# Kernel optimization log

Hardware: AMD Instinct MI355X
Metric: run time of the kernel (lower is better)

## Reference

```python
import jax, jax.numpy as jnp
import numpy as np

B, N, C = 4, 262144, 10
K_PRE, K_POST = 4096, 500          # before_nms_max, after_nms_max
ROI_THR, NMS_THR = 0.1, 0.01       # roi_threshold, nms_threshold


def setup_inputs() -> dict:
    key = jax.random.key(0)
    k1, k2, k3, k4 = jax.random.split(key, 4)
    # raw logits; sigmoid(-2 + noise) straddles roi_threshold=0.1 realistically
    cls = jax.random.normal(k1, (B, N, C), jnp.float32) - 2.0
    centers = jax.random.uniform(k2, (B, N, 3), jnp.float32, minval=-50.0, maxval=50.0)
    sizes = jax.random.uniform(k3, (B, N, 3), jnp.float32, minval=0.5, maxval=5.0)
    heading = jax.random.uniform(k4, (B, N, 1), jnp.float32, minval=-np.pi, maxval=np.pi)
    boxes = jnp.concatenate([centers, sizes, heading], axis=-1)  # (B, N, 7)
    return {"batch_cls_preds": cls, "batch_box_preds": boxes}


def _pairwise_bev_iou(b):
    # b: (K, 7) = [x, y, z, dx, dy, dz, heading]; BEV IoU (heading ignored,
    # axis-aligned approximation of the rotated-IoU CUDA kernel).
    x, y, dx, dy = b[:, 0], b[:, 1], b[:, 3], b[:, 4]
    x1, x2 = x - dx * 0.5, x + dx * 0.5
    y1, y2 = y - dy * 0.5, y + dy * 0.5
    ix = jnp.clip(jnp.minimum(x2[:, None], x2[None, :]) - jnp.maximum(x1[:, None], x1[None, :]), 0.0)
    iy = jnp.clip(jnp.minimum(y2[:, None], y2[None, :]) - jnp.maximum(y1[:, None], y1[None, :]), 0.0)
    inter = ix * iy                              # (K, K)
    area = dx * dy                               # (K,)
    union = area[:, None] + area[None, :] - inter
    return inter / jnp.maximum(union, 1e-6)


def _nms_one(scores, labels, boxes):
    # scores: (N,), labels: (N,) int32, boxes: (N, 7)
    s = jnp.where(scores > ROI_THR, scores, -1.0)       # score-threshold filter
    topv, topi = jax.lax.top_k(s, K_PRE)                # keep top before_nms_max
    tb = boxes[topi]                                     # (K_PRE, 7)
    tl = labels[topi]
    iou = _pairwise_bev_iou(tb)                          # (K_PRE, K_PRE)
    keep0 = topv > ROI_THR

    def body(i, keep):
        # a kept higher-score box i suppresses later boxes with IoU > thr
        sup = (iou[i] > NMS_THR) & (jnp.arange(K_PRE) > i) & keep[i]
        return keep & ~sup

    keep = jax.lax.fori_loop(0, K_PRE, body, keep0)
    kept_scores = jnp.where(keep, topv, -1.0)
    fv, fi = jax.lax.top_k(kept_scores, K_POST)          # after_nms_max slots
    m = fv > 0.0
    final_scores = jnp.where(m, fv, 0.0)                 # (K_POST,)
    final_boxes = tb[fi] * m[:, None].astype(tb.dtype)   # (K_POST, 7)
    final_labels = jnp.where(m, tl[fi], -1)              # (K_POST,)
    return final_scores, final_boxes, final_labels


def reference(batch_cls_preds, batch_box_preds):
    probs = jax.nn.sigmoid(batch_cls_preds)              # (B, N, C)
    scores = jnp.max(probs, axis=-1)                     # per-anchor best class score
    labels = jnp.argmax(probs, axis=-1).astype(jnp.int32)
    final_scores, final_boxes, final_labels = jax.vmap(_nms_one)(scores, labels, batch_box_preds)
    return final_scores, final_boxes, final_labels
```

## Files before the change

### kernel.cpp

```cpp
#include <hip/hip_runtime.h>
#include <stdint.h>

constexpr int B = 4;
constexpr int N = 262144;
constexpr int C = 10;
constexpr int KPRE = 4096;
constexpr int KPOST = 500;
constexpr float ROI_THR = 0.1f;
constexpr float NMS_THR = 0.01f;
constexpr int CAP = 8192;
constexpr int MASKW = KPRE / 64;
constexpr int RJT = 2;

__device__ __forceinline__ uint32_t f2k(float f) {
  uint32_t u = __float_as_uint(f);
  return (u & 0x80000000u) ? ~u : (u | 0x80000000u);
}
__device__ __forceinline__ float k2f(uint32_t k) {
  uint32_t u = (k & 0x80000000u) ? (k ^ 0x80000000u) : ~k;
  return __uint_as_float(u);
}
__device__ __forceinline__ float sigm(float x) { return 1.0f / (1.0f + expf(-x)); }

__device__ __forceinline__ void async_lds16(const void* g, void* l) {
  __builtin_amdgcn_global_load_lds((const __attribute__((address_space(1))) void*)g,
                                   (__attribute__((address_space(3))) void*)l, 16, 0, 0);
}

__device__ __forceinline__ uint2 select256(const uint32_t* __restrict__ h, uint32_t R,
                                           uint32_t* s, uint32_t* o2) {
  int t = threadIdx.x;
  s[t] = h[t];
  __syncthreads();
  for (int off = 1; off < 256; off <<= 1) {
    uint32_t v = s[t] + ((t + off < 256) ? s[t + off] : 0u);
    __syncthreads();
    s[t] = v;
    __syncthreads();
  }
  uint32_t suf = s[t];
  uint32_t sufn = (t < 255) ? s[t + 1] : 0u;
  if (suf >= R && R > sufn) {
    o2[0] = (uint32_t)t;
    o2[1] = R - sufn;
  }
  __syncthreads();
  uint2 r;
  r.x = o2[0];
  r.y = o2[1];
  __syncthreads();
  return r;
}

__global__ void scoreK(const float* __restrict__ cls, uint32_t* __restrict__ keys,
                       uint32_t* __restrict__ hist0) {
  __shared__ float ls[2560];
  __shared__ uint32_t h[256];
  int b = blockIdx.y;
  int t = threadIdx.x;
  h[t] = 0;
  size_t base = ((size_t)b * N + (size_t)blockIdx.x * 256) * C;
  const float2* g2 = (const float2*)(cls + base);
  float2* l2 = (float2*)ls;
#pragma unroll
  for (int r = 0; r < 5; ++r) l2[r * 256 + t] = g2[r * 256 + t];
  __syncthreads();
  const float* mine = ls + t * 10;
  float m = mine[0];
#pragma unroll
  for (int c = 1; c < C; ++c) m = fmaxf(m, mine[c]);
  float p = sigm(m);
  float sc = (p > ROI_THR) ? p : -1.0f;
  uint32_t k = f2k(sc);
  keys[(size_t)b * N + blockIdx.x * 256 + t] = k;
  atomicAdd(&h[k >> 24], 1u);
  __syncthreads();
  if (h[t]) atomicAdd(&hist0[b * 256 + t], h[t]);
}

__global__ void histP1K(const uint32_t* __restrict__ keys, const uint32_t* __restrict__ hist0,
                        uint32_t* __restrict__ hist1) {
  __shared__ uint32_t s[256];
  __shared__ uint32_t o2[2];
  __shared__ uint32_t h[256];
  int b = blockIdx.y;
  int t = threadIdx.x;
  uint2 s0 = select256(hist0 + b * 256, (uint32_t)KPRE, s, o2);
  h[t] = 0;
  __syncthreads();
  uint32_t pref = s0.x;
  const uint4* kb4 = (const uint4*)(keys + (size_t)b * N);
#pragma unroll
  for (int r = 0; r < 2; ++r) {
    uint4 kv = kb4[blockIdx.x * 512 + r * 256 + t];
#pragma unroll
    for (int j = 0; j < 4; ++j) {
      uint32_t k = (&kv.x)[j];
      if ((k >> 24) == pref) atomicAdd(&h[(k >> 16) & 255u], 1u);
    }
  }
  __syncthreads();
  if (h[t]) atomicAdd(&hist1[b * 256 + t], h[t]);
}

__global__ void compactK(const uint32_t* __restrict__ keys, const uint32_t* __restrict__ hist0,
                         const uint32_t* __restrict__ hist1, unsigned long long* __restrict__ list,
                         uint32_t* __restrict__ cnt) {
  __shared__ uint32_t s[256];
  __shared__ uint32_t o2[2];
  __shared__ uint32_t scan[256];
  __shared__ uint32_t baseSh;
  int b = blockIdx.y;
  int t = threadIdx.x;
  uint2 s0 = select256(hist0 + b * 256, (uint32_t)KPRE, s, o2);
  uint2 s1 = select256(hist1 + b * 256, s0.y, s, o2);
  uint32_t T = ((s0.x << 8) | s1.x) << 16;
  const uint4* kb4 = (const uint4*)(keys + (size_t)b * N);
  uint4 kv[4];
#pragma unroll
  for (int r = 0; r < 4; ++r) kv[r] = kb4[blockIdx.x * 1024 + r * 256 + t];
  uint32_t c = 0;
#pragma unroll
  for (int r = 0; r < 4; ++r)
#pragma unroll
    for (int j = 0; j < 4; ++j) c += ((&kv[r].x)[j] >= T) ? 1u : 0u;
  scan[t] = c;
  __syncthreads();
  for (int off = 1; off < 256; off <<= 1) {
    uint32_t v = scan[t] + ((t >= off) ? scan[t - off] : 0u);
    __syncthreads();
    scan[t] = v;
    __syncthreads();
  }
  uint32_t excl = scan[t] - c;
  if (t == 255) baseSh = atomicAdd(&cnt[b], scan[255]);
  __syncthreads();
  uint32_t pos = baseSh + excl;
#pragma unroll
  for (int r = 0; r < 4; ++r)
#pragma unroll
    for (int j = 0; j < 4; ++j) {
      uint32_t k = (&kv[r].x)[j];
      if (k >= T) {
        uint32_t n = (blockIdx.x * 1024 + r * 256 + t) * 4 + j;
        if (pos < CAP)
          list[(size_t)b * CAP + pos] = ((unsigned long long)k << 32) | (uint32_t)(~n);
        pos++;
      }
    }
}

__global__ void rankK(const unsigned long long* __restrict__ list, const uint32_t* __restrict__ cnt,
                      uint32_t* __restrict__ rank) {
  __shared__ unsigned long long lp[256];
  int b = blockIdx.z;
  int cc = (int)min(cnt[b], (uint32_t)CAP);
  if (blockIdx.x * 256 >= cc) return;
  int j0 = blockIdx.y * (256 * RJT);
  if (j0 >= cc) return;
  int i = blockIdx.x * 256 + threadIdx.x;
  unsigned long long pi = (i < cc) ? list[(size_t)b * CAP + i] : ~0ull;
  uint32_t c = 0;
#pragma unroll
  for (int tb = 0; tb < RJT; ++tb) {
    int j = j0 + tb * 256 + threadIdx.x;
    __syncthreads();
    lp[threadIdx.x] = (j < cc) ? list[(size_t)b * CAP + j] : 0ull;
    __syncthreads();
#pragma unroll 8
    for (int jj = 0; jj < 256; ++jj) c += (lp[jj] > pi) ? 1u : 0u;
  }
  if (i < cc && c) atomicAdd(&rank[(size_t)b * CAP + i], c);
}

__global__ void scatterK(const unsigned long long* __restrict__ list,
                         const uint32_t* __restrict__ cnt, const uint32_t* __restrict__ rank,
                         const float* __restrict__ boxes, float* __restrict__ sel_score,
                         uint32_t* __restrict__ sel_idx, float* __restrict__ sel_box) {
  int b = blockIdx.y;
  int p = blockIdx.x * 256 + threadIdx.x;
  uint32_t cc = min(cnt[b], (uint32_t)CAP);
  if (p >= (int)cc) return;
  unsigned long long pk = list[(size_t)b * CAP + p];
  uint32_t r = rank[(size_t)b * CAP + p];
  if (r >= (uint32_t)KPRE) return;
  uint32_t key = (uint32_t)(pk >> 32);
  uint32_t idx = ~(uint32_t)pk;
  sel_score[b * KPRE + r] = k2f(key);
  sel_idx[b * KPRE + r] = idx;
  const float* src = boxes + ((size_t)b * N + idx) * 7;
  float* dst = sel_box + ((size_t)b * KPRE + r) * 8;
#pragma unroll
  for (int c = 0; c < 7; ++c) dst[c] = src[c];
  dst[7] = 0.f;
}

__global__ void maskK(const float* __restrict__ sel_box, unsigned long long* __restrict__ mask) {
  int b = blockIdx.z;
  int bi = blockIdx.x;
  int w = blockIdx.y;
  int t = threadIdx.x;
  int i = bi * 256 + t;
  int j0 = w * 64;
  unsigned long long* dst = mask + ((size_t)b * KPRE + i) * MASKW + w;
  if (j0 + 63 <= bi * 256) {
    *dst = 0ull;
    return;
  }
  __shared__ float4 jv[64];
  __shared__ float ja[64];
  if (t < 64) {
    const float4* bj = (const float4*)(sel_box + ((size_t)b * KPRE + j0 + t) * 8);
    float4 lo = bj[0], hi = bj[1];
    float xj = lo.x, yj = lo.y, dxj = lo.w, dyj = hi.x;
    float hxj = __fmul_rn(dxj, 0.5f), hyj = __fmul_rn(dyj, 0.5f);
    float4 v;
    v.x = __fsub_rn(xj, hxj);
    v.y = __fadd_rn(xj, hxj);
    v.z = __fsub_rn(yj, hyj);
    v.w = __fadd_rn(yj, hyj);
    jv[t] = v;
    ja[t] = __fmul_rn(dxj, dyj);
  }
  __syncthreads();
  const float4* myb = (const float4*)(sel_box + ((size_t)b * KPRE + i) * 8);
  float4 lo = myb[0], hi = myb[1];
  float x = lo.x, y = lo.y, dx = lo.w, dy = hi.x;
  float hx = __fmul_rn(dx, 0.5f), hy = __fmul_rn(dy, 0.5f);
  float x1i = __fsub_rn(x, hx), x2i = __fadd_rn(x, hx);
  float y1i = __fsub_rn(y, hy), y2i = __fadd_rn(y, hy);
  float ai = __fmul_rn(dx, dy);
  unsigned long long wacc = 0ull;
#pragma unroll 16
  for (int jj = 0; jj < 64; ++jj) {
    int j = j0 + jj;
    float4 v = jv[jj];
    float aj = ja[jj];
    float xx1 = fmaxf(x1i, v.x);
    float xx2 = fminf(x2i, v.y);
    float yy1 = fmaxf(y1i, v.z);
    float yy2 = fminf(y2i, v.w);
    float ix = fmaxf(__fsub_rn(xx2, xx1), 0.0f);
    float iy = fmaxf(__fsub_rn(yy2, yy1), 0.0f);
    float inter = __fmul_rn(ix, iy);
    float den = fmaxf(__fsub_rn(__fadd_rn(ai, aj), inter), 1e-6f);
    float q0 = __fmul_rn(NMS_THR, den);
    float d = __fsub_rn(inter, q0);
    bool sup = d > 0.0f;
    if (__builtin_expect(__any(fabsf(d) <= q0 * 1e-5f), 0)) {
      sup = (inter / den) > NMS_THR;
    }
    sup = sup && (j > i);
    wacc |= ((unsigned long long)(sup ? 1u : 0u)) << jj;
  }
  *dst = wacc;
}

__global__ void transK(const unsigned long long* __restrict__ mask,
                       unsigned long long* __restrict__ Tmat) {
  int b = blockIdx.y;
  int g = blockIdx.x;
  int t = threadIdx.x;
  unsigned long long m = mask[((size_t)b * KPRE + g * 64 + t) * MASKW + g];
  unsigned long long T = 0ull;
#pragma unroll
  for (int j = 0; j < 64; ++j) {
    unsigned long long bj = __ballot(((m >> j) & 1ull) != 0ull);
    if (t == j) T = bj;
  }
  Tmat[((size_t)b * 64 + g) * 128 + t] = T;
  Tmat[((size_t)b * 64 + g) * 128 + 64 + t] = m;
}

__global__ void nmsK(const unsigned long long* __restrict__ mask,
                     const unsigned long long* __restrict__ Tmat,
                     const float* __restrict__ sel_score,
                     uint32_t* __restrict__ kept_pos, uint32_t* __restrict__ kept_cnt) {
  __shared__ unsigned long long lds[3][64][64];
  __shared__ unsigned long long tl[3][128];
  __shared__ uint32_t keptbuf[KPOST];
  int b = blockIdx.x;
  int t = threadIdx.x;

  unsigned long long cand = 0ull;
  for (int k = 0; k < 64; ++k) {
    float s = sel_score[b * KPRE + k * 64 + t];
    unsigned long long bal = __ballot(s > ROI_THR);
    if (t == k) cand = bal;
  }

  const unsigned long long* mb = mask + (size_t)b * KPRE * MASKW;
  const unsigned long long* tb = Tmat + (size_t)b * 64 * 128;
  unsigned long long remv = 0ull;
  int kc = 0;

  auto prefetch = [&](int g2, int buf2) {
    const char* base = (const char*)(mb + (size_t)g2 * 64 * MASKW);
#pragma unroll
    for (int p = 0; p < 32; ++p)
      async_lds16(base + (size_t)p * 1024 + (size_t)t * 16, &lds[buf2][p * 2][0]);
    async_lds16((const char*)(tb + (size_t)g2 * 128) + (size_t)t * 16, &tl[buf2][0]);
  };

  prefetch(0, 0);
  prefetch(1, 1);
  for (int g = 0; g < 64; ++g) {
    int buf = g % 3;
    if (g < 63) {
      asm volatile("s_waitcnt vmcnt(33)" ::: "memory");
    } else {
      asm volatile("s_waitcnt vmcnt(0)" ::: "memory");
    }
    if (g + 2 < 64) {
      asm volatile("s_waitcnt lgkmcnt(0)" ::: "memory");
      prefetch(g + 2, (g + 2) % 3);
    }

    unsigned long long cw = cand & ~remv;
    unsigned long long aw =
        ((unsigned long long)(uint32_t)__builtin_amdgcn_readlane((uint32_t)(cw >> 32), g) << 32) |
        (uint32_t)__builtin_amdgcn_readlane((uint32_t)cw, g);
    if (aw) {
      unsigned long long T = tl[buf][t];
      unsigned long long m = tl[buf][64 + t];
      unsigned long long K = __ballot((m & aw) != 0ull);
      unsigned long long alive = aw;
      unsigned long long rem = aw & K;
      if (rem) {
        bool deadf = ((aw >> t) & 1ull) == 0ull;
        while (rem) {
          int s = __ffsll((long long)rem) - 1;
          rem &= rem - 1ull;
          if ((alive >> s) & 1ull) {
            deadf = deadf || (((T >> s) & 1ull) != 0ull);
            alive = __ballot(!deadf);
            rem &= alive;
          }
        }
      }
      int grp = __popcll(alive);
      if ((alive >> t) & 1ull) {
        int rk = __popcll(alive & ((1ull << t) - 1ull));
        if (kc + rk < KPOST) keptbuf[kc + rk] = (uint32_t)(g * 64 + t);
      }
      unsigned long long acc = 0ull, a2 = alive;
      while (a2) {
        int s2 = __ffsll((long long)a2) - 1;
        a2 &= a2 - 1ull;
        acc |= lds[buf][s2][t];
      }
      remv |= acc;
      kc += grp;
      if (kc >= KPOST) break;
    }
  }
  asm volatile("s_waitcnt vmcnt(0)" ::: "memory");
  int kcc = min(kc, KPOST);
  for (int i = t; i < kcc; i += 64) kept_pos[b * KPOST + i] = keptbuf[i];
  if (t == 0) kept_cnt[b] = (uint32_t)kcc;
}

__global__ void outK(const float* __restrict__ cls,
                     const float* __restrict__ sel_score, const uint32_t* __restrict__ sel_idx,
                     const float* __restrict__ sel_box,
                     const uint32_t* __restrict__ kept_pos, const uint32_t* __restrict__ kept_cnt,
                     float* __restrict__ out) {
  int b = blockIdx.y;
  int s = blockIdx.x * blockDim.x + threadIdx.x;
  if (s >= KPOST) return;
  float* oS = out;
  float* oB = out + B * KPOST;
  float* oL = out + B * KPOST + B * KPOST * 7;
  uint32_t kcnt = kept_cnt[b];
  if (s < (int)kcnt) {
    uint32_t pos = kept_pos[b * KPOST + s];
    oS[b * KPOST + s] = sel_score[b * KPRE + pos];
    const float* box = sel_box + ((size_t)b * KPRE + pos) * 8;
    float* dst = oB + ((size_t)b * KPOST + s) * 7;
#pragma unroll
    for (int c = 0; c < 7; ++c) dst[c] = box[c];
    uint32_t idx = sel_idx[b * KPRE + pos];
    const float* p = cls + ((size_t)b * N + idx) * C;
    float bestv = sigm(p[0]);
    int bestc = 0;
#pragma unroll
    for (int c = 1; c < C; ++c) {
      float v = sigm(p[c]);
      if (v > bestv) { bestv = v; bestc = c; }
    }
    oL[b * KPOST + s] = (float)bestc;
  } else {
    oS[b * KPOST + s] = 0.0f;
    float* dst = oB + ((size_t)b * KPOST + s) * 7;
#pragma unroll
    for (int c = 0; c < 7; ++c) dst[c] = 0.0f;
    oL[b * KPOST + s] = -1.0f;
  }
}

__global__ void sentinelK(float* out, int n) {
  int i = blockIdx.x * blockDim.x + threadIdx.x;
  if (i < n) out[i] = 1337.0f;
}

extern "C" void kernel_launch(void* const* d_in, const int* in_sizes, int n_in,
                              void* d_out, int out_size, void* d_ws, size_t ws_size,
                              hipStream_t stream) {
  const float* cls = (const float*)d_in[0];
  const float* boxes = (const float*)d_in[1];
  float* out = (float*)d_out;

  char* ws = (char*)d_ws;
  size_t off = 0;
  auto alloc = [&](size_t bytes) -> void* {
    void* p = ws + off;
    off = (off + bytes + 255) & ~(size_t)255;
    return p;
  };
  unsigned long long* mask = (unsigned long long*)alloc((size_t)B * KPRE * MASKW * 8);
  unsigned long long* list = (unsigned long long*)alloc((size_t)B * CAP * 8);
  uint32_t* keys = (uint32_t*)alloc((size_t)B * N * 4);
  float* sel_box = (float*)alloc((size_t)B * KPRE * 8 * 4);
  float* sel_score = (float*)alloc((size_t)B * KPRE * 4);
  uint32_t* sel_idx = (uint32_t*)alloc((size_t)B * KPRE * 4);
  uint32_t* kept_pos = (uint32_t*)alloc((size_t)B * KPOST * 4);
  uint32_t* kept_cnt = (uint32_t*)alloc(B * 4);
  unsigned long long* Tmat = (unsigned long long*)alloc((size_t)B * 64 * 128 * 8);

  uint32_t* hist0 = (uint32_t*)mask;
  uint32_t* hist1 = hist0 + B * 256;
  uint32_t* cnt = hist1 + B * 256;
  uint32_t* rank = (uint32_t*)((char*)mask + 16384);
  size_t zbytes = 16384 + (size_t)B * CAP * 4;

  if (off > ws_size) {
    sentinelK<<<dim3((out_size + 255) / 256), 256, 0, stream>>>(out, out_size);
    return;
  }

  hipMemsetAsync(mask, 0, zbytes, stream);
  scoreK<<<dim3(N / 256, B), 256, 0, stream>>>(cls, keys, hist0);
  histP1K<<<dim3(N / 2048, B), 256, 0, stream>>>(keys, hist0, hist1);
  compactK<<<dim3(N / 4096, B), 256, 0, stream>>>(keys, hist0, hist1, list, cnt);
  rankK<<<dim3(CAP / 256, CAP / (256 * RJT), B), 256, 0, stream>>>(list, cnt, rank);
  scatterK<<<dim3(CAP / 256, B), 256, 0, stream>>>(list, cnt, rank, boxes, sel_score, sel_idx,
                                                   sel_box);
  maskK<<<dim3(16, 64, B), 256, 0, stream>>>(sel_box, mask);
  transK<<<dim3(64, B), 64, 0, stream>>>(mask, Tmat);
  nmsK<<<B, 64, 0, stream>>>(mask, Tmat, sel_score, kept_pos, kept_cnt);
  outK<<<dim3((KPOST + 255) / 256, B), 256, 0, stream>>>(cls, sel_score, sel_idx, sel_box,
                                                         kept_pos, kept_cnt, out);
}
```

Baseline: 158.2 us.

## Fuse diagonal transpose into mask kernel and defer NMS row loads into registers

The separate transpose kernel is removed: the mask kernel block that owns each diagonal 64x64 tile now builds the transposed tile with ballots and writes it to Tmat directly. The NMS kernel preloads all diagonal tiles into LDS up front. It replaces the triple-buffered LDS prefetch of whole 64-row mask groups with direct global loads of only the rows of surviving boxes. Those loads go into up to 32 registers and are OR-reduced at the start of the next group, so their latency overlaps the next group's work. This drops one launch and avoids moving unused mask rows. In exchange the serial NMS loop now waits on global-load latency, and the 32-entry register array raises register pressure.

```diff
diff --git a/kernel.cpp b/kernel.cpp
--- a/kernel.cpp
+++ b/kernel.cpp
@@ -11,6 +11,7 @@
 constexpr int CAP = 8192;
 constexpr int MASKW = KPRE / 64;
 constexpr int RJT = 2;
+constexpr int MAXP = 32;
 
 __device__ __forceinline__ uint32_t f2k(float f) {
   uint32_t u = __float_as_uint(f);
@@ -195,7 +196,8 @@
   dst[7] = 0.f;
 }
 
-__global__ void maskK(const float* __restrict__ sel_box, unsigned long long* __restrict__ mask) {
+__global__ void maskK(const float* __restrict__ sel_box, unsigned long long* __restrict__ mask,
+                      unsigned long long* __restrict__ Tmat) {
   int b = blockIdx.z;
   int bi = blockIdx.x;
   int w = blockIdx.y;
@@ -254,33 +256,33 @@
     wacc |= ((unsigned long long)(sup ? 1u : 0u)) << jj;
   }
   *dst = wacc;
-}
-
-__global__ void transK(const unsigned long long* __restrict__ mask,
-                       unsigned long long* __restrict__ Tmat) {
-  int b = blockIdx.y;
-  int g = blockIdx.x;
-  int t = threadIdx.x;
-  unsigned long long m = mask[((size_t)b * KPRE + g * 64 + t) * MASKW + g];
-  unsigned long long T = 0ull;
-#pragma unroll
-  for (int j = 0; j < 64; ++j) {
-    unsigned long long bj = __ballot(((m >> j) & 1ull) != 0ull);
-    if (t == j) T = bj;
-  }
-  Tmat[((size_t)b * 64 + g) * 128 + t] = T;
-  Tmat[((size_t)b * 64 + g) * 128 + 64 + t] = m;
+  if ((w >> 2) == bi && (t >> 6) == (w & 3)) {
+    int l = t & 63;
+    unsigned long long m = wacc;
+    unsigned long long T = 0ull;
+#pragma unroll
+    for (int j = 0; j < 64; ++j) {
+      unsigned long long bj = __ballot(((m >> j) & 1ull) != 0ull);
+      if (l == j) T = bj;
+    }
+    unsigned long long* trow = Tmat + ((size_t)b * 64 + w) * 128;
+    trow[l] = T;
+    trow[64 + l] = m;
+  }
 }
 
 __global__ void nmsK(const unsigned long long* __restrict__ mask,
                      const unsigned long long* __restrict__ Tmat,
                      const float* __restrict__ sel_score,
                      uint32_t* __restrict__ kept_pos, uint32_t* __restrict__ kept_cnt) {
-  __shared__ unsigned long long lds[3][64][64];
-  __shared__ unsigned long long tl[3][128];
+  __shared__ unsigned long long td[64][128];
   __shared__ uint32_t keptbuf[KPOST];
   int b = blockIdx.x;
   int t = threadIdx.x;
+
+  const char* tsrc = (const char*)(Tmat + (size_t)b * 64 * 128);
+  for (int g = 0; g < 64; ++g)
+    async_lds16(tsrc + (size_t)g * 1024 + (size_t)t * 16, &td[g][0]);
 
   unsigned long long cand = 0ull;
   for (int k = 0; k < 64; ++k) {
@@ -288,41 +290,26 @@
     unsigned long long bal = __ballot(s > ROI_THR);
     if (t == k) cand = bal;
   }
+  asm volatile("s_waitcnt vmcnt(0)" ::: "memory");
 
   const unsigned long long* mb = mask + (size_t)b * KPRE * MASKW;
-  const unsigned long long* tb = Tmat + (size_t)b * 64 * 128;
   unsigned long long remv = 0ull;
+  unsigned long long r[MAXP];
+#pragma unroll
+  for (int a = 0; a < MAXP; ++a) r[a] = 0ull;
   int kc = 0;
 
-  auto prefetch = [&](int g2, int buf2) {
-    const char* base = (const char*)(mb + (size_t)g2 * 64 * MASKW);
-#pragma unroll
-    for (int p = 0; p < 32; ++p)
-      async_lds16(base + (size_t)p * 1024 + (size_t)t * 16, &lds[buf2][p * 2][0]);
-    async_lds16((const char*)(tb + (size_t)g2 * 128) + (size_t)t * 16, &tl[buf2][0]);
-  };
-
-  prefetch(0, 0);
-  prefetch(1, 1);
   for (int g = 0; g < 64; ++g) {
-    int buf = g % 3;
-    if (g < 63) {
-      asm volatile("s_waitcnt vmcnt(33)" ::: "memory");
-    } else {
-      asm volatile("s_waitcnt vmcnt(0)" ::: "memory");
-    }
-    if (g + 2 < 64) {
-      asm volatile("s_waitcnt lgkmcnt(0)" ::: "memory");
-      prefetch(g + 2, (g + 2) % 3);
-    }
+#pragma unroll
+    for (int a = 0; a < MAXP; ++a) remv |= r[a];
 
     unsigned long long cw = cand & ~remv;
     unsigned long long aw =
         ((unsigned long long)(uint32_t)__builtin_amdgcn_readlane((uint32_t)(cw >> 32), g) << 32) |
         (uint32_t)__builtin_amdgcn_readlane((uint32_t)cw, g);
     if (aw) {
-      unsigned long long T = tl[buf][t];
-      unsigned long long m = tl[buf][64 + t];
+      unsigned long long T = td[g][t];
+      unsigned long long m = td[g][64 + t];
       unsigned long long K = __ballot((m & aw) != 0ull);
       unsigned long long alive = aw;
       unsigned long long rem = aw & K;
@@ -343,15 +330,35 @@
         int rk = __popcll(alive & ((1ull << t) - 1ull));
         if (kc + rk < KPOST) keptbuf[kc + rk] = (uint32_t)(g * 64 + t);
       }
-      unsigned long long acc = 0ull, a2 = alive;
-      while (a2) {
-        int s2 = __ffsll((long long)a2) - 1;
-        a2 &= a2 - 1ull;
-        acc |= lds[buf][s2][t];
+      kc += grp;
+      unsigned long long a2 = alive;
+      bool again = true;
+      while (again) {
+#pragma unroll
+        for (int a = 0; a < MAXP; ++a) {
+          if (a2) {
+            int s2 = __ffsll((long long)a2) - 1;
+            a2 &= a2 - 1ull;
+            r[a] = mb[(size_t)(g * 64 + s2) * MASKW + t];
+          } else {
+            r[a] = 0ull;
+          }
+        }
+        if (a2) {
+#pragma unroll
+          for (int a = 0; a < MAXP; ++a) {
+            remv |= r[a];
+            r[a] = 0ull;
+          }
+          again = true;
+        } else {
+          again = false;
+        }
       }
-      remv |= acc;
-      kc += grp;
       if (kc >= KPOST) break;
+    } else {
+#pragma unroll
+      for (int a = 0; a < MAXP; ++a) r[a] = 0ull;
     }
   }
   asm volatile("s_waitcnt vmcnt(0)" ::: "memory");
@@ -445,8 +452,7 @@
   rankK<<<dim3(CAP / 256, CAP / (256 * RJT), B), 256, 0, stream>>>(list, cnt, rank);
   scatterK<<<dim3(CAP / 256, B), 256, 0, stream>>>(list, cnt, rank, boxes, sel_score, sel_idx,
                                                    sel_box);
-  maskK<<<dim3(16, 64, B), 256, 0, stream>>>(sel_box, mask);
-  transK<<<dim3(64, B), 64, 0, stream>>>(mask, Tmat);
+  maskK<<<dim3(16, 64, B), 256, 0, stream>>>(sel_box, mask, Tmat);
   nmsK<<<B, 64, 0, stream>>>(mask, Tmat, sel_score, kept_pos, kept_cnt);
   outK<<<dim3((KPOST + 255) / 256, B), 256, 0, stream>>>(cls, sel_score, sel_idx, sel_box,
                                                          kept_pos, kept_cnt, out);
```

Measured after the change: 142.5 us. 9.9% less time.
